# Optimization experiments

Hardware: AMD Instinct MI355X
Metric: run time of the kernel (lower is better)

Reference implementation:

```python
import jax, jax.numpy as jnp
import numpy as np

TEMP = 0.1
EPS = 1e-12  # F.normalize eps


def setup_inputs() -> dict:
    key = jax.random.key(0)
    k1, k2 = jax.random.split(key)
    B, C, N = 8, 128, 4096
    features = jax.random.normal(k1, (B, C, N), dtype=jnp.float32)
    labels_all = jax.random.randint(k2, (B, N), 0, 16, dtype=jnp.int32)
    return {"features": features, "labels_all": labels_all}


def _per_cloud_loss(features_map, labels):
    # features_map: [C, N], labels: [N]
    v = features_map.T  # [N, C]
    v = v / jnp.maximum(jnp.linalg.norm(v, axis=1, keepdims=True), EPS)
    dp = jnp.exp(jnp.matmul(v, v.T) / TEMP)  # [N, N]
    n = dp.shape[0]
    # remove diagonal (dot_products - diag(diagonal))
    dp = dp * (1.0 - jnp.eye(n, dtype=dp.dtype))
    mask = labels[:, None] == labels[None, :]  # [N, N]
    positives = jnp.sum(jnp.where(mask, dp, 0.0), axis=1)
    negatives = jnp.sum(jnp.where(mask, 0.0, dp), axis=1)
    deviation = -jnp.log(positives / (positives + negatives))
    return jnp.mean(deviation)


def reference(features, labels_all):
    # features: [B, C, N], labels_all: [B, N]
    losses = jax.vmap(_per_cloud_loss)(features, labels_all)  # [B]
    return jnp.mean(losses)
```

## Files before the change

kernel.cpp:

```cpp
#include <hip/hip_runtime.h>
#include <hip/hip_bf16.h>
#include <math.h>

#define BATCH 8
#define NPTS 4096
#define CH 128

#define SQRT_TEMP_LOG2E 3.79828256f

typedef __attribute__((ext_vector_type(4))) float f32x4;
typedef __attribute__((ext_vector_type(4))) int   i32x4;
typedef __attribute__((ext_vector_type(8))) short bf16x8;

typedef __attribute__((address_space(3))) unsigned int lds_uint;
typedef __attribute__((address_space(1))) const unsigned int gbl_uint;

__device__ __forceinline__ void load_lds16(const void* g, const void* l) {
    __builtin_amdgcn_global_load_lds((gbl_uint*)g, (lds_uint*)l, 16, 0, 0);
}

__device__ __forceinline__ float fast_exp2(float x) {
    return __builtin_amdgcn_exp2f(x);
}

__global__ __launch_bounds__(256) void normalize_kernel(
    const float* __restrict__ f, __hip_bfloat16* __restrict__ vn,
    float* __restrict__ pos, float* __restrict__ neg)
{
    int idx = blockIdx.x * 256 + threadIdx.x;
    int point = idx >> 2, q = idx & 3;
    int b = point >> 12, n = point & (NPTS - 1);
    const float* base = f + (size_t)b * CH * NPTS + (size_t)(q * 32) * NPTS + n;

    float x[32];
    float ss = 0.0f;
    #pragma unroll
    for (int c = 0; c < 32; c++) {
        x[c] = base[(size_t)c * NPTS];
        ss += x[c] * x[c];
    }
    ss += __shfl_xor(ss, 1);
    ss += __shfl_xor(ss, 2);
    float scale = SQRT_TEMP_LOG2E / fmaxf(sqrtf(ss), 1e-12f);

    __hip_bfloat16* out = vn + (size_t)point * CH + q * 32;
    #pragma unroll
    for (int c0 = 0; c0 < 32; c0 += 8) {
        union { __hip_bfloat16 h[8]; uint4 u; } pk;
        #pragma unroll
        for (int j = 0; j < 8; j++)
            pk.h[j] = __float2bfloat16(x[c0 + j] * scale);
        *((uint4*)(out + c0)) = pk.u;
    }
    if (q == 0) pos[point] = 0.0f;
    else if (q == 1) neg[point] = 0.0f;
}

__global__ __launch_bounds__(256, 4) void tile_kernel(
    const __hip_bfloat16* __restrict__ vn, const int* __restrict__ labels,
    float* __restrict__ pos, float* __restrict__ neg)
{
    __shared__ short lB[128 * CH];
    __shared__ int labC[128];

    const int b  = blockIdx.z;
    const int rt = blockIdx.y, ct = blockIdx.x;
    const bool diag = (rt == ct);

    const int tid = threadIdx.x;
    const int w = tid >> 6, lane = tid & 63;
    const int lane15 = lane & 15, quad = lane >> 4;

    const int row0 = rt * 128, col0 = ct * 128;
    const __hip_bfloat16* vb = vn + (size_t)b * NPTS * CH;

    if (tid < 128) labC[tid] = labels[b * NPTS + col0 + tid];

    {
        const __hip_bfloat16* Bb = vb + (size_t)col0 * CH;
        #pragma unroll
        for (int i = 0; i < 8; i++) {
            int ldsrow = (w * 8 + i) * 4;
            int r = ldsrow + quad;
            int g = lane15 ^ (r & 15);
            load_lds16(Bb + (size_t)r * CH + g * 8, &lB[ldsrow * CH]);
        }
    }

    bf16x8 afrag[2][4];
    int lr[2];
    #pragma unroll
    for (int mi = 0; mi < 2; mi++) {
        const int row_l = w * 32 + mi * 16 + lane15;
        const __hip_bfloat16* Arow = vb + (size_t)(row0 + row_l) * CH;
        #pragma unroll
        for (int ks = 0; ks < 4; ks++)
            afrag[mi][ks] = *(const bf16x8*)(Arow + (ks * 4 + quad) * 8);
        lr[mi] = labels[b * NPTS + row0 + row_l];
    }

    __syncthreads();

    f32x4 acc[2][8] = {};
    #pragma unroll
    for (int ks = 0; ks < 4; ks++) {
        const int koff = ((ks * 4 + quad) ^ lane15) << 3;
        #pragma unroll
        for (int ni = 0; ni < 8; ni++) {
            bf16x8 bf = *(const bf16x8*)&lB[(ni * 16 + lane15) * CH + koff];
            acc[0][ni] = __builtin_amdgcn_mfma_f32_16x16x32_bf16(
                bf, afrag[0][ks], acc[0][ni], 0, 0, 0);
            acc[1][ni] = __builtin_amdgcn_mfma_f32_16x16x32_bf16(
                bf, afrag[1][ks], acc[1][ni], 0, 0, 0);
        }
    }

    #pragma unroll
    for (int mi = 0; mi < 2; mi++) {
        const int row_l = w * 32 + mi * 16 + lane15;
        float p = 0.0f, tt = 0.0f;
        if (diag) {
            #pragma unroll
            for (int ni = 0; ni < 8; ni++) {
                const bool dblk = (ni * 16 == w * 32 + mi * 16);
                const i32x4 lc = *(const i32x4*)&labC[ni * 16 + quad * 4];
                #pragma unroll
                for (int r = 0; r < 4; r++) {
                    float e = fast_exp2(acc[mi][ni][r]);
                    if (dblk && lane15 == quad * 4 + r) e = 0.0f;
                    tt += e;
                    p  += (lc[r] == lr[mi]) ? e : 0.0f;
                }
            }
        } else {
            #pragma unroll
            for (int ni = 0; ni < 8; ni++) {
                const i32x4 lc = *(const i32x4*)&labC[ni * 16 + quad * 4];
                #pragma unroll
                for (int r = 0; r < 4; r++) {
                    float e = fast_exp2(acc[mi][ni][r]);
                    tt += e;
                    p  += (lc[r] == lr[mi]) ? e : 0.0f;
                }
            }
        }
        p  += __shfl_xor(p, 16);   p  += __shfl_xor(p, 32);
        tt += __shfl_xor(tt, 16);  tt += __shfl_xor(tt, 32);
        if (lane < 16) {
            atomicAdd(&pos[b * NPTS + row0 + row_l], p);
            atomicAdd(&neg[b * NPTS + row0 + row_l], tt - p);
        }
    }
}

__global__ __launch_bounds__(1024) void finalize_kernel(
    const float* __restrict__ pos, const float* __restrict__ neg,
    float* __restrict__ out)
{
    float acc = 0.0f;
    for (int i = threadIdx.x; i < BATCH * NPTS; i += 1024) {
        float p = pos[i];
        float t = p + neg[i];
        acc += __logf(t / p);
    }
    #pragma unroll
    for (int off = 32; off; off >>= 1) acc += __shfl_down(acc, off);
    __shared__ float red[16];
    if ((threadIdx.x & 63) == 0) red[threadIdx.x >> 6] = acc;
    __syncthreads();
    if (threadIdx.x < 16) {
        float v = red[threadIdx.x];
        #pragma unroll
        for (int off = 8; off; off >>= 1) v += __shfl_down(v, off);
        if (threadIdx.x == 0) out[0] = v * (1.0f / (BATCH * NPTS));
    }
}

extern "C" void kernel_launch(void* const* d_in, const int* in_sizes, int n_in,
                              void* d_out, int out_size, void* d_ws, size_t ws_size,
                              hipStream_t stream)
{
    const float* features = (const float*)d_in[0];
    const int*   labels   = (const int*)d_in[1];
    float*       out      = (float*)d_out;

    __hip_bfloat16* vn = (__hip_bfloat16*)d_ws;
    float* pos = (float*)((char*)d_ws + (size_t)BATCH * NPTS * CH * sizeof(__hip_bfloat16));
    float* neg = pos + BATCH * NPTS;

    hipLaunchKernelGGL(normalize_kernel, dim3(BATCH * NPTS * 4 / 256), dim3(256), 0, stream,
                       features, vn, pos, neg);
    hipLaunchKernelGGL(tile_kernel, dim3(32, 32, BATCH), dim3(256), 0, stream,
                       vn, labels, pos, neg);
    hipLaunchKernelGGL(finalize_kernel, dim3(1), dim3(1024), 0, stream, pos, neg, out);
}
```

Baseline: 125.5 us.

## Loop over column chunks per block with double-buffered LDS and parallel finalize

Each tile block now keeps its A fragments in registers and walks a quarter of the columns in 64-column chunks. The next chunk is prefetched into a second LDS buffer while MFMAs run on the current one, and pos/neg are accumulated in registers before one atomic per row. This cuts global atomics by a factor of eight, avoids reloading A per tile, and overlaps loads with compute, at the cost of far fewer blocks (1024 vs 8192). The finalize kernel is spread over 32 blocks that atomically add into an output zeroed in the normalize kernel.

Measured after the change: 118.6 us. 5.4% less time.

```diff
diff --git a/kernel.cpp b/kernel.cpp
--- a/kernel.cpp
+++ b/kernel.cpp
@@ -5,6 +5,9 @@
 #define BATCH 8
 #define NPTS 4096
 #define CH 128
+#define CTG 4
+#define CHUNK 64
+#define NCHUNK (NPTS / (CTG * CHUNK))
 
 #define SQRT_TEMP_LOG2E 3.79828256f
 
@@ -25,7 +28,7 @@
 
 __global__ __launch_bounds__(256) void normalize_kernel(
     const float* __restrict__ f, __hip_bfloat16* __restrict__ vn,
-    float* __restrict__ pos, float* __restrict__ neg)
+    float* __restrict__ pos, float* __restrict__ neg, float* __restrict__ out)
 {
     int idx = blockIdx.x * 256 + threadIdx.x;
     int point = idx >> 2, q = idx & 3;
@@ -43,49 +46,50 @@
     ss += __shfl_xor(ss, 2);
     float scale = SQRT_TEMP_LOG2E / fmaxf(sqrtf(ss), 1e-12f);
 
-    __hip_bfloat16* out = vn + (size_t)point * CH + q * 32;
+    __hip_bfloat16* outp = vn + (size_t)point * CH + q * 32;
     #pragma unroll
     for (int c0 = 0; c0 < 32; c0 += 8) {
         union { __hip_bfloat16 h[8]; uint4 u; } pk;
         #pragma unroll
         for (int j = 0; j < 8; j++)
             pk.h[j] = __float2bfloat16(x[c0 + j] * scale);
-        *((uint4*)(out + c0)) = pk.u;
+        *((uint4*)(outp + c0)) = pk.u;
     }
     if (q == 0) pos[point] = 0.0f;
     else if (q == 1) neg[point] = 0.0f;
+    if (idx == 0) out[0] = 0.0f;
 }
 
 __global__ __launch_bounds__(256, 4) void tile_kernel(
     const __hip_bfloat16* __restrict__ vn, const int* __restrict__ labels,
     float* __restrict__ pos, float* __restrict__ neg)
 {
-    __shared__ short lB[128 * CH];
-    __shared__ int labC[128];
-
-    const int b  = blockIdx.z;
-    const int rt = blockIdx.y, ct = blockIdx.x;
-    const bool diag = (rt == ct);
-
+    __shared__ short lB[2][CHUNK * CH];
+    __shared__ int labL[NPTS / CTG];
+
+    const int ctg = blockIdx.x, rt = blockIdx.y, b = blockIdx.z;
     const int tid = threadIdx.x;
     const int w = tid >> 6, lane = tid & 63;
     const int lane15 = lane & 15, quad = lane >> 4;
 
-    const int row0 = rt * 128, col0 = ct * 128;
+    const int row0 = rt * 128;
+    const int colbase = ctg * (NPTS / CTG);
     const __hip_bfloat16* vb = vn + (size_t)b * NPTS * CH;
-
-    if (tid < 128) labC[tid] = labels[b * NPTS + col0 + tid];
-
-    {
-        const __hip_bfloat16* Bb = vb + (size_t)col0 * CH;
-        #pragma unroll
-        for (int i = 0; i < 8; i++) {
-            int ldsrow = (w * 8 + i) * 4;
+    const int* labb = labels + b * NPTS;
+
+    auto STAGE = [&](int buf, int chunk) {
+        const __hip_bfloat16* Bb = vb + (size_t)(colbase + chunk * CHUNK) * CH;
+        #pragma unroll
+        for (int i = 0; i < 4; i++) {
+            int ldsrow = w * 16 + i * 4;
             int r = ldsrow + quad;
             int g = lane15 ^ (r & 15);
-            load_lds16(Bb + (size_t)r * CH + g * 8, &lB[ldsrow * CH]);
-        }
-    }
+            load_lds16(Bb + (size_t)r * CH + g * 8, &lB[buf][ldsrow * CH]);
+        }
+    };
+
+    load_lds16(labb + colbase + w * 256 + lane * 4, &labL[w * 256]);
+    STAGE(0, 0);
 
     bf16x8 afrag[2][4];
     int lr[2];
@@ -96,83 +100,100 @@
         #pragma unroll
         for (int ks = 0; ks < 4; ks++)
             afrag[mi][ks] = *(const bf16x8*)(Arow + (ks * 4 + quad) * 8);
-        lr[mi] = labels[b * NPTS + row0 + row_l];
-    }
-
-    __syncthreads();
-
-    f32x4 acc[2][8] = {};
-    #pragma unroll
-    for (int ks = 0; ks < 4; ks++) {
-        const int koff = ((ks * 4 + quad) ^ lane15) << 3;
-        #pragma unroll
-        for (int ni = 0; ni < 8; ni++) {
-            bf16x8 bf = *(const bf16x8*)&lB[(ni * 16 + lane15) * CH + koff];
-            acc[0][ni] = __builtin_amdgcn_mfma_f32_16x16x32_bf16(
-                bf, afrag[0][ks], acc[0][ni], 0, 0, 0);
-            acc[1][ni] = __builtin_amdgcn_mfma_f32_16x16x32_bf16(
-                bf, afrag[1][ks], acc[1][ni], 0, 0, 0);
-        }
-    }
-
-    #pragma unroll
-    for (int mi = 0; mi < 2; mi++) {
-        const int row_l = w * 32 + mi * 16 + lane15;
-        float p = 0.0f, tt = 0.0f;
-        if (diag) {
+        lr[mi] = labb[row0 + row_l];
+    }
+
+    float pacc[2] = {0.0f, 0.0f}, tacc[2] = {0.0f, 0.0f};
+
+    auto BODY = [&](int chunk, int buf) {
+        STAGE(buf ^ 1, (chunk + 1) & (NCHUNK - 1));
+        asm volatile("s_waitcnt vmcnt(4)" ::: "memory");
+        __builtin_amdgcn_s_barrier();
+
+        f32x4 acc[2][4] = {};
+        __builtin_amdgcn_s_setprio(1);
+        #pragma unroll
+        for (int ks = 0; ks < 4; ks++) {
+            const int koff = ((ks * 4 + quad) ^ lane15) << 3;
             #pragma unroll
-            for (int ni = 0; ni < 8; ni++) {
-                const bool dblk = (ni * 16 == w * 32 + mi * 16);
-                const i32x4 lc = *(const i32x4*)&labC[ni * 16 + quad * 4];
-                #pragma unroll
-                for (int r = 0; r < 4; r++) {
-                    float e = fast_exp2(acc[mi][ni][r]);
-                    if (dblk && lane15 == quad * 4 + r) e = 0.0f;
-                    tt += e;
-                    p  += (lc[r] == lr[mi]) ? e : 0.0f;
+            for (int ni = 0; ni < 4; ni++) {
+                bf16x8 bf = *(const bf16x8*)&lB[buf][(ni * 16 + lane15) * CH + koff];
+                acc[0][ni] = __builtin_amdgcn_mfma_f32_16x16x32_bf16(
+                    bf, afrag[0][ks], acc[0][ni], 0, 0, 0);
+                acc[1][ni] = __builtin_amdgcn_mfma_f32_16x16x32_bf16(
+                    bf, afrag[1][ks], acc[1][ni], 0, 0, 0);
+            }
+        }
+        __builtin_amdgcn_s_setprio(0);
+        __builtin_amdgcn_s_barrier();
+
+        #pragma unroll
+        for (int ni = 0; ni < 4; ni++) {
+            const i32x4 lc = *(const i32x4*)&labL[chunk * CHUNK + ni * 16 + quad * 4];
+            const int colblk = colbase + chunk * CHUNK + ni * 16;
+            #pragma unroll
+            for (int mi = 0; mi < 2; mi++) {
+                const bool dblk = (colblk == row0 + w * 32 + mi * 16);
+                if (dblk) {
+                    #pragma unroll
+                    for (int r = 0; r < 4; r++) {
+                        float e = fast_exp2(acc[mi][ni][r]);
+                        if (lane15 == quad * 4 + r) e = 0.0f;
+                        tacc[mi] += e;
+                        pacc[mi] += (lc[r] == lr[mi]) ? e : 0.0f;
+                    }
+                } else {
+                    #pragma unroll
+                    for (int r = 0; r < 4; r++) {
+                        float e = fast_exp2(acc[mi][ni][r]);
+                        tacc[mi] += e;
+                        pacc[mi] += (lc[r] == lr[mi]) ? e : 0.0f;
+                    }
                 }
             }
-        } else {
-            #pragma unroll
-            for (int ni = 0; ni < 8; ni++) {
-                const i32x4 lc = *(const i32x4*)&labC[ni * 16 + quad * 4];
-                #pragma unroll
-                for (int r = 0; r < 4; r++) {
-                    float e = fast_exp2(acc[mi][ni][r]);
-                    tt += e;
-                    p  += (lc[r] == lr[mi]) ? e : 0.0f;
-                }
-            }
-        }
+        }
+    };
+
+    #pragma unroll 1
+    for (int c2 = 0; c2 < NCHUNK; c2 += 2) {
+        BODY(c2, 0);
+        BODY(c2 + 1, 1);
+    }
+
+    #pragma unroll
+    for (int mi = 0; mi < 2; mi++) {
+        float p = pacc[mi], tt = tacc[mi];
         p  += __shfl_xor(p, 16);   p  += __shfl_xor(p, 32);
         tt += __shfl_xor(tt, 16);  tt += __shfl_xor(tt, 32);
         if (lane < 16) {
+            const int row_l = w * 32 + mi * 16 + lane15;
             atomicAdd(&pos[b * NPTS + row0 + row_l], p);
             atomicAdd(&neg[b * NPTS + row0 + row_l], tt - p);
         }
     }
 }
 
-__global__ __launch_bounds__(1024) void finalize_kernel(
+__global__ __launch_bounds__(256) void finalize_kernel(
     const float* __restrict__ pos, const float* __restrict__ neg,
     float* __restrict__ out)
 {
+    int base = blockIdx.x * 1024 + threadIdx.x;
     float acc = 0.0f;
-    for (int i = threadIdx.x; i < BATCH * NPTS; i += 1024) {
+    #pragma unroll
+    for (int k = 0; k < 4; k++) {
+        int i = base + k * 256;
         float p = pos[i];
         float t = p + neg[i];
         acc += __logf(t / p);
     }
     #pragma unroll
     for (int off = 32; off; off >>= 1) acc += __shfl_down(acc, off);
-    __shared__ float red[16];
+    __shared__ float red[4];
     if ((threadIdx.x & 63) == 0) red[threadIdx.x >> 6] = acc;
     __syncthreads();
-    if (threadIdx.x < 16) {
-        float v = red[threadIdx.x];
-        #pragma unroll
-        for (int off = 8; off; off >>= 1) v += __shfl_down(v, off);
-        if (threadIdx.x == 0) out[0] = v * (1.0f / (BATCH * NPTS));
+    if (threadIdx.x == 0) {
+        float v = red[0] + red[1] + red[2] + red[3];
+        atomicAdd(out, v * (1.0f / (BATCH * NPTS)));
     }
 }
 
@@ -189,8 +210,8 @@
     float* neg = pos + BATCH * NPTS;
 
     hipLaunchKernelGGL(normalize_kernel, dim3(BATCH * NPTS * 4 / 256), dim3(256), 0, stream,
-                       features, vn, pos, neg);
-    hipLaunchKernelGGL(tile_kernel, dim3(32, 32, BATCH), dim3(256), 0, stream,
+                       features, vn, pos, neg, out);
+    hipLaunchKernelGGL(tile_kernel, dim3(CTG, 32, BATCH), dim3(256), 0, stream,
                        vn, labels, pos, neg);
-    hipLaunchKernelGGL(finalize_kernel, dim3(1), dim3(1024), 0, stream, pos, neg, out);
-}
+    hipLaunchKernelGGL(finalize_kernel, dim3(32), dim3(256), 0, stream, pos, neg, out);
+}
```
